# Performance work log

Measured on AMD Instinct MI355X. Metric: run time of the kernel, lower is better.

The kernel has to match this reference:

```python
import jax, jax.numpy as jnp
import numpy as np

N = 50000      # nodes
E = 800000     # edges (avg degree 16)
D_IN, D_H, D_OUT = 128, 256, 128


def setup_inputs() -> dict:
    key = jax.random.key(0)
    ks = jax.random.split(key, 12)
    x = jax.random.normal(ks[0], (N, D_IN), jnp.float32)
    src = jax.random.randint(ks[1], (E,), 0, N)
    dst = jax.random.randint(ks[2], (E,), 0, N)

    def lin(k, din, dout):
        return (jax.random.normal(k, (din, dout), jnp.float32) / np.sqrt(din)).astype(jnp.float32)

    dims = [(D_IN, D_H), (D_H, D_H), (D_H, D_OUT)]
    params = {}
    ki = 3
    for i, (di, do) in enumerate(dims):
        params[f"W_self{i}"] = lin(ks[ki], di, do); ki += 1
        params[f"W_neigh{i}"] = lin(ks[ki], di, do); ki += 1
        params[f"b{i}"] = jnp.zeros((do,), jnp.float32)
    return {"x": x, "src": src, "dst": dst, **params}


def _mean_agg(h, src, dst):
    # gather src features along edges, segment-mean into dst nodes
    msg = jnp.take(h, src, axis=0)                              # [E, D]
    s = jax.ops.segment_sum(msg, dst, num_segments=N)           # [N, D]
    deg = jax.ops.segment_sum(jnp.ones((dst.shape[0], 1), h.dtype), dst, num_segments=N)
    return s / jnp.maximum(deg, 1.0)                            # zero-degree -> 0, as in DGL


def reference(x, src, dst,
              W_self0, W_neigh0, b0,
              W_self1, W_neigh1, b1,
              W_self2, W_neigh2, b2):
    Ws = [(W_self0, W_neigh0, b0), (W_self1, W_neigh1, b1), (W_self2, W_neigh2, b2)]
    h = x
    for i, (Ws_i, Wn_i, b_i) in enumerate(Ws):
        neigh = _mean_agg(h, src, dst)
        h = h @ Ws_i + neigh @ Wn_i + b_i                       # SAGEConv('mean')
        if i < len(Ws) - 1:
            h = jax.nn.relu(h)                                  # activation between layers
    return h
```

## Files before the change

kernel.cpp:

```cpp
#include <hip/hip_runtime.h>

#define NN 50000
#define NE 800000
#define NCHK 200
#define CHKE 4000
#define NBUK 196
#define BCAP 5120
#define NOFF (NBUK * NCHK)
#define NSB  ((NOFF + 255) / 256)

typedef __attribute__((ext_vector_type(8))) short short8;
typedef __attribute__((ext_vector_type(4))) float f32x4;
typedef unsigned int u32;
typedef unsigned short u16;

__device__ __forceinline__ float bf2f(short u) {
    union { unsigned int i; float f; } c;
    c.i = ((unsigned int)(unsigned short)u) << 16;
    return c.f;
}
__device__ __forceinline__ short f2bf(float f) {
    union { float f; unsigned int i; } c; c.f = f;
    unsigned int u = c.i;
    unsigned int r = (u + 0x7FFFu + ((u >> 16) & 1u)) >> 16;
    return (short)r;
}


__global__ void cvt_f32_bf16_kernel(const float* __restrict__ in, short* __restrict__ out, int n) {
    int gid = blockIdx.x * 256 + threadIdx.x;
    if (gid < n) out[gid] = f2bf(in[gid]);
}

__global__ void wcvt_all_kernel(const float* __restrict__ Ws0, const float* __restrict__ Wn0,
                                const float* __restrict__ Ws1, const float* __restrict__ Wn1,
                                const float* __restrict__ Ws2, const float* __restrict__ Wn2,
                                short* __restrict__ wts) {
    int gid = blockIdx.x * 256 + threadIdx.x;
    const float* W; int K, Dout, base, loc;
    if (gid < 65536)       { K = 128; Dout = 256; base = (gid < 32768)  ? 0 : 32768;
                             W = (gid < 32768)  ? Ws0 : Wn0; loc = gid & 32767; }
    else if (gid < 196608) { K = 256; Dout = 256; base = (gid < 131072) ? 65536 : 131072;
                             W = (gid < 131072) ? Ws1 : Wn1; loc = (gid - 65536) & 65535; }
    else                   { K = 256; Dout = 128; base = (gid < 229376) ? 196608 : 229376;
                             W = (gid < 229376) ? Ws2 : Wn2; loc = (gid - 196608) & 32767; }
    int k = loc / Dout, d = loc - k * Dout;
    int kt = k >> 6, ks = (k >> 5) & 1, kg = (k >> 3) & 3, j = k & 7;
    int cgp = d >> 4, l = d & 15;
    int off = ((((kt * 2 + ks) * (Dout >> 4) + cgp) * 4 + kg) * 16 + l) * 8 + j;
    wts[base + off] = f2bf(W[(long)k * Dout + d]);
}

__global__ __launch_bounds__(256) void bucket_hist_kernel(const int* __restrict__ dst,
                                                          int* __restrict__ chist) {
    __shared__ int lh[NBUK];
    int b = blockIdx.x, t = threadIdx.x;
    for (int i = t; i < NBUK; i += 256) lh[i] = 0;
    __syncthreads();
    int base = b * CHKE;
    for (int i = t; i < CHKE; i += 256) atomicAdd(&lh[dst[base + i] >> 8], 1);
    __syncthreads();
    for (int i = t; i < NBUK; i += 256) chist[i * NCHK + b] = lh[i];
}

__global__ __launch_bounds__(256) void off_blocksum_kernel(const int* __restrict__ in,
                                                           int* __restrict__ bsum) {
    __shared__ int sm[256];
    int t = threadIdx.x;
    int idx = blockIdx.x * 256 + t;
    sm[t] = (idx < NOFF) ? in[idx] : 0;
    __syncthreads();
    for (int off = 128; off > 0; off >>= 1) {
        if (t < off) sm[t] += sm[t + off];
        __syncthreads();
    }
    if (t == 0) bsum[blockIdx.x] = sm[0];
}

__global__ __launch_bounds__(256) void off_scanb_kernel(const int* __restrict__ bsum,
                                                        int* __restrict__ bpre) {
    __shared__ int sm[256];
    int t = threadIdx.x;
    sm[t] = (t < NSB) ? bsum[t] : 0;
    __syncthreads();
    for (int o = 1; o < 256; o <<= 1) {
        int v = sm[t];
        int a = (t >= o) ? sm[t - o] : 0;
        __syncthreads();
        sm[t] = v + a;
        __syncthreads();
    }
    if (t < NSB) bpre[t] = (t == 0) ? 0 : sm[t - 1];
}

__global__ __launch_bounds__(256) void off_scatter_kernel(const int* __restrict__ in,
                                                          const int* __restrict__ bpre,
                                                          int* __restrict__ off) {
    __shared__ int sm[256];
    int t = threadIdx.x;
    int idx = blockIdx.x * 256 + t;
    int val = (idx < NOFF) ? in[idx] : 0;
    sm[t] = val;
    __syncthreads();
    for (int o = 1; o < 256; o <<= 1) {
        int v = sm[t];
        int a = (t >= o) ? sm[t - o] : 0;
        __syncthreads();
        sm[t] = v + a;
        __syncthreads();
    }
    if (idx < NOFF) off[idx] = bpre[blockIdx.x] + sm[t] - val;
}

__global__ __launch_bounds__(256) void bucket_scatter_kernel(const int* __restrict__ src,
                                                             const int* __restrict__ dst,
                                                             const int* __restrict__ off,
                                                             u32* __restrict__ ebuf) {
    __shared__ int lcur[NBUK];
    int b = blockIdx.x, t = threadIdx.x;
    for (int i = t; i < NBUK; i += 256) lcur[i] = off[i * NCHK + b];
    __syncthreads();
    int base = b * CHKE;
    for (int i = t; i < CHKE; i += 256) {
        int d = dst[base + i], s = src[base + i];
        int slot = atomicAdd(&lcur[d >> 8], 1);
        ebuf[slot] = ((u32)(d & 255) << 16) | (u32)s;
    }
}

__global__ __launch_bounds__(256) void bucket_sort_kernel(const u32* __restrict__ ebuf,
                                                          const int* __restrict__ off,
                                                          u16* __restrict__ srcs16,
                                                          int* __restrict__ row_start,
                                                          int* __restrict__ cnt) {
    __shared__ u32 earr[BCAP];
    __shared__ u16 s16[BCAP];
    __shared__ int lhist[256], lpre[256], lcur[256];
    int k = blockIdx.x, t = threadIdx.x;
    int base = off[k * NCHK];
    int end  = (k < NBUK - 1) ? off[(k + 1) * NCHK] : NE;
    int nE = end - base;
    lhist[t] = 0;
    __syncthreads();
    for (int i = t; i < nE; i += 256) {
        u32 e = ebuf[base + i];
        earr[i] = e;
        atomicAdd(&lhist[e >> 16], 1);
    }
    __syncthreads();
    int v = lhist[t];
    lpre[t] = v;
    __syncthreads();
    for (int o = 1; o < 256; o <<= 1) {
        int x = lpre[t];
        int a = (t >= o) ? lpre[t - o] : 0;
        __syncthreads();
        lpre[t] = x + a;
        __syncthreads();
    }
    int excl = lpre[t] - v;
    int node = k * 256 + t;
    if (node < NN) { row_start[node] = base + excl; cnt[node] = v; }
    lcur[t] = excl;
    __syncthreads();
    for (int i = t; i < nE; i += 256) {
        u32 e = earr[i];
        int pos = atomicAdd(&lcur[e >> 16], 1);
        s16[pos] = (u16)(e & 0xFFFFu);
    }
    __syncthreads();
    for (int i = t; i < nE; i += 256) srcs16[base + i] = s16[i];
}


template<int D>
__global__ __launch_bounds__(256) void gather_mean2_kernel(
    const short* __restrict__ h, const u16* __restrict__ srcs,
    const int* __restrict__ row_start, const int* __restrict__ cnt,
    short* __restrict__ nb)
{
    constexpr int CPR = D / 8;
    constexpr int EPL = 64 / CPR;
    const int wave = threadIdx.x >> 6;
    const int lane = threadIdx.x & 63;
    const int v = blockIdx.x * 4 + wave;
    if (v >= NN) return;
    const int c  = cnt[v];
    const int rs = row_start[v];
    const int slot = lane / CPR;
    const int cg   = lane & (CPR - 1);
    float acc[8];
    #pragma unroll
    for (int j = 0; j < 8; ++j) acc[j] = 0.f;
    const short8* hp = (const short8*)h;
    int i = slot;
    for (; i + 3 * EPL < c; i += 4 * EPL) {
        int s0 = srcs[rs + i];
        int s1 = srcs[rs + i + EPL];
        int s2 = srcs[rs + i + 2 * EPL];
        int s3 = srcs[rs + i + 3 * EPL];
        short8 v0 = hp[(size_t)s0 * CPR + cg];
        short8 v1 = hp[(size_t)s1 * CPR + cg];
        short8 v2 = hp[(size_t)s2 * CPR + cg];
        short8 v3 = hp[(size_t)s3 * CPR + cg];
        #pragma unroll
        for (int j = 0; j < 8; ++j)
            acc[j] += (bf2f(v0[j]) + bf2f(v1[j])) + (bf2f(v2[j]) + bf2f(v3[j]));
    }
    for (; i < c; i += EPL) {
        int s0 = srcs[rs + i];
        short8 v0 = hp[(size_t)s0 * CPR + cg];
        #pragma unroll
        for (int j = 0; j < 8; ++j) acc[j] += bf2f(v0[j]);
    }
    #pragma unroll
    for (int j = 0; j < 8; ++j) {
        if (EPL == 4) acc[j] += __shfl_xor(acc[j], 16);
        acc[j] += __shfl_xor(acc[j], 32);
    }
    if (slot == 0) {
        float inv = (c > 0) ? (1.0f / (float)c) : 0.0f;
        short8 outv;
        #pragma unroll
        for (int j = 0; j < 8; ++j) outv[j] = f2bf(acc[j] * inv);
        ((short8*)nb)[(size_t)v * CPR + cg] = outv;
    }
}

template<int NOUT, int KK, int PHASES, bool RELU, bool OUT_F32, bool ADDIN, bool BIAS>
__global__ __launch_bounds__(512, 2) void gemm_sage4_kernel(
    const short* __restrict__ Aself, const short* __restrict__ Aneigh,
    const short* __restrict__ Bself, const short* __restrict__ Bneigh,
    const float* __restrict__ bias, void* __restrict__ outp, int M,
    const short* __restrict__ addin)
{
    constexpr int WN = NOUT / 64;
    constexpr int WM = 8 / WN;
    constexpr int MR = 128 / (WM * 16);
    constexpr int NR = 4;
    constexpr int KT = KK / 64;
    constexpr int NT = PHASES * KT;
    constexpr int CG = NOUT / 16;

    __shared__ short ldsA[2][128 * 64];

    const int tid  = threadIdx.x;
    const int wave = tid >> 6;
    const int lane = tid & 63;
    const int wm = wave / WN;
    const int wn = wave % WN;
    const int l15 = lane & 15;
    const int kg  = lane >> 4;
    const int bm  = blockIdx.x * 128;

    f32x4 acc[MR][NR];
    #pragma unroll
    for (int a = 0; a < MR; ++a)
        #pragma unroll
        for (int b = 0; b < NR; ++b)
            acc[a][b] = (f32x4){0.f, 0.f, 0.f, 0.f};

    const int srow = tid >> 3;
    const int scol = ((tid & 7) << 3) ^ ((srow & 7) << 3);

    auto stageA = [&](int buf, int t) {
        int ph = t / KT, kt = t - ph * KT;
        const short* A = ph ? Aneigh : Aself;
        #pragma unroll
        for (int c = 0; c < 2; ++c) {
            const short* gp = A + (size_t)(bm + c * 64 + srow) * KK + kt * 64 + scol;
            __builtin_amdgcn_global_load_lds(
                (const __attribute__((address_space(1))) u32*)gp,
                (__attribute__((address_space(3))) u32*)(&ldsA[buf][c * 4096 + (wave << 9)]),
                16, 0, 0);
        }
    };

    stageA(0, 0);
    __syncthreads();

    #pragma unroll
    for (int ph = 0; ph < PHASES; ++ph) {
        const short* __restrict__ Wb = ph ? Bneigh : Bself;
        short8 wreg[KT][2][NR];
        #pragma unroll
        for (int kt = 0; kt < KT; ++kt)
            #pragma unroll
            for (int ks = 0; ks < 2; ++ks)
                #pragma unroll
                for (int nr = 0; nr < NR; ++nr)
                    wreg[kt][ks][nr] = *(const short8*)(
                        Wb + (size_t)((((kt * 2 + ks) * CG + wn * 4 + nr) * 4 + kg) * 16 + l15) * 8);

        #pragma unroll
        for (int kt = 0; kt < KT; ++kt) {
            const int t = ph * KT + kt;
            const int cur = t & 1;
            if (t + 1 < NT) stageA(cur ^ 1, t + 1);

            #pragma unroll
            for (int ks = 0; ks < 2; ++ks) {
                short8 areg[MR];
                #pragma unroll
                for (int mr = 0; mr < MR; ++mr) {
                    int r = wm * (MR * 16) + mr * 16 + l15;
                    areg[mr] = *(const short8*)(&ldsA[cur][r * 64 + ((ks * 32 + kg * 8) ^ ((r & 7) << 3))]);
                }
                #pragma unroll
                for (int mr = 0; mr < MR; ++mr)
                    #pragma unroll
                    for (int nr = 0; nr < NR; ++nr)
                        acc[mr][nr] = __builtin_amdgcn_mfma_f32_16x16x32_bf16(
                            areg[mr], wreg[kt][ks][nr], acc[mr][nr], 0, 0, 0);
            }
            __syncthreads();
        }
    }

    #pragma unroll
    for (int mr = 0; mr < MR; ++mr) {
        int rowb = bm + wm * (MR * 16) + mr * 16 + kg * 4;
        #pragma unroll
        for (int nr = 0; nr < NR; ++nr) {
            int col = wn * 64 + nr * 16 + l15;
            float bv = BIAS ? bias[col] : 0.f;
            #pragma unroll
            for (int r = 0; r < 4; ++r) {
                int row = rowb + r;
                if (row < M) {
                    float vv = acc[mr][nr][r] + bv;
                    if (ADDIN) vv += bf2f(addin[(size_t)row * NOUT + col]);
                    if (RELU) vv = fmaxf(vv, 0.f);
                    if (OUT_F32) ((float*)outp)[(size_t)row * NOUT + col] = vv;
                    else         ((short*)outp)[(size_t)row * NOUT + col] = f2bf(vv);
                }
            }
        }
    }
}


extern "C" void kernel_launch(void* const* d_in, const int* in_sizes, int n_in,
                              void* d_out, int out_size, void* d_ws, size_t ws_size,
                              hipStream_t stream) {
    const float* x    = (const float*)d_in[0];
    const int*   srcp = (const int*)d_in[1];
    const int*   dstp = (const int*)d_in[2];
    const float* Ws0  = (const float*)d_in[3];
    const float* Wn0  = (const float*)d_in[4];
    const float* b0   = (const float*)d_in[5];
    const float* Ws1  = (const float*)d_in[6];
    const float* Wn1  = (const float*)d_in[7];
    const float* b1   = (const float*)d_in[8];
    const float* Ws2  = (const float*)d_in[9];
    const float* Wn2  = (const float*)d_in[10];
    const float* b2   = (const float*)d_in[11];

    char* base = (char*)d_ws;
    size_t off_b = 0;
    auto alloc = [&](size_t bytes) -> void* {
        void* p = base + off_b;
        off_b += (bytes + 255) & ~(size_t)255;
        return p;
    };

    int*   cnt       = (int*)alloc((size_t)NN * 4);
    int*   row_start = (int*)alloc((size_t)NN * 4);
    int*   chist     = (int*)alloc((size_t)NOFF * 4);
    int*   offb      = (int*)alloc((size_t)NOFF * 4);
    int*   bsum      = (int*)alloc((size_t)NSB * 4);
    int*   bpre      = (int*)alloc((size_t)NSB * 4);
    u32*   ebuf      = (u32*)alloc((size_t)NE * 4);
    u16*   srcs16    = (u16*)alloc((size_t)NE * 2);
    short* hA        = (short*)alloc((size_t)NN * 256 * 2);
    short* hB        = (short*)alloc((size_t)NN * 256 * 2);
    short* nb        = (short*)alloc((size_t)NN * 256 * 2);
    short* wts       = (short*)alloc((size_t)262144 * 2 + 65536);
    short* Wt0s = wts;
    short* Wt0n = Wt0s + 32768;
    short* Wt1s = Wt0n + 32768;
    short* Wt1n = Wt1s + 65536;
    short* Wt2s = Wt1n + 65536;
    short* Wt2n = Wt2s + 32768;

    bucket_hist_kernel<<<NCHK, 256, 0, stream>>>(dstp, chist);
    off_blocksum_kernel<<<NSB, 256, 0, stream>>>(chist, bsum);
    off_scanb_kernel<<<1, 256, 0, stream>>>(bsum, bpre);
    off_scatter_kernel<<<NSB, 256, 0, stream>>>(chist, bpre, offb);
    bucket_scatter_kernel<<<NCHK, 256, 0, stream>>>(srcp, dstp, offb, ebuf);
    bucket_sort_kernel<<<NBUK, 256, 0, stream>>>(ebuf, offb, srcs16, row_start, cnt);

    wcvt_all_kernel<<<1024, 256, 0, stream>>>(Ws0, Wn0, Ws1, Wn1, Ws2, Wn2, wts);

    cvt_f32_bf16_kernel<<<(NN * 128 + 255) / 256, 256, 0, stream>>>(x, hA, NN * 128);

    const int mblocks = (NN + 127) / 128;
    const int gblocks = (NN + 3) / 4;

    gather_mean2_kernel<128><<<gblocks, 256, 0, stream>>>(hA, srcs16, row_start, cnt, nb);
    gemm_sage4_kernel<256, 128, 2, true, false, false, true><<<mblocks, 512, 0, stream>>>(
        hA, nb, Wt0s, Wt0n, b0, hB, NN, nullptr);

    gather_mean2_kernel<256><<<gblocks, 256, 0, stream>>>(hB, srcs16, row_start, cnt, nb);
    gemm_sage4_kernel<256, 256, 2, true, false, false, true><<<mblocks, 512, 0, stream>>>(
        hB, nb, Wt1s, Wt1n, b1, hA, NN, nullptr);

    gemm_sage4_kernel<128, 256, 1, false, false, false, false><<<mblocks, 512, 0, stream>>>(
        hA, hA, Wt2n, Wt2n, nullptr, hB, NN, nullptr);
    gather_mean2_kernel<128><<<gblocks, 256, 0, stream>>>(hB, srcs16, row_start, cnt, nb);
    gemm_sage4_kernel<128, 256, 1, false, true, true, true><<<mblocks, 512, 0, stream>>>(
        hA, hA, Wt2s, Wt2s, b2, d_out, NN, nb);
}
```

Baseline: 246.8 us.

## Shrink GEMM blocks to 256 threads and stream weight fragments per k-step

The SAGE GEMM drops from 512-thread, 128-row tiles to 256-thread tiles (64 rows for the 256-wide layers, 128 rows for the 128-wide ones). Each wave now always computes a 4x4 MFMA tile. Weight fragments are no longer preloaded in registers for a whole phase; they are loaded from global memory for each k-step inside a single flat loop over phases. The aim is to cut register pressure and raise occupancy (launch bounds 256,4). The cost is more repeated weight loads from cache and, for the 256-wide layers, twice as many blocks that each re-read the weights.

```diff
diff --git a/kernel.cpp b/kernel.cpp
--- a/kernel.cpp
+++ b/kernel.cpp
@@ -228,21 +228,23 @@
 }
 
 template<int NOUT, int KK, int PHASES, bool RELU, bool OUT_F32, bool ADDIN, bool BIAS>
-__global__ __launch_bounds__(512, 2) void gemm_sage4_kernel(
+__global__ __launch_bounds__(256, 4) void gemm_sage5_kernel(
     const short* __restrict__ Aself, const short* __restrict__ Aneigh,
     const short* __restrict__ Bself, const short* __restrict__ Bneigh,
     const float* __restrict__ bias, void* __restrict__ outp, int M,
     const short* __restrict__ addin)
 {
     constexpr int WN = NOUT / 64;
-    constexpr int WM = 8 / WN;
-    constexpr int MR = 128 / (WM * 16);
+    constexpr int WM = 4 / WN;
+    constexpr int BM = 64 * WM;
+    constexpr int SC = BM / 32;
+    constexpr int MR = 4;
     constexpr int NR = 4;
     constexpr int KT = KK / 64;
     constexpr int NT = PHASES * KT;
     constexpr int CG = NOUT / 16;
 
-    __shared__ short ldsA[2][128 * 64];
+    __shared__ short ldsA[2][BM * 64];
 
     const int tid  = threadIdx.x;
     const int wave = tid >> 6;
@@ -251,7 +253,7 @@
     const int wn = wave % WN;
     const int l15 = lane & 15;
     const int kg  = lane >> 4;
-    const int bm  = blockIdx.x * 128;
+    const int bm  = blockIdx.x * BM;
 
     f32x4 acc[MR][NR];
     #pragma unroll
@@ -267,11 +269,11 @@
         int ph = t / KT, kt = t - ph * KT;
         const short* A = ph ? Aneigh : Aself;
         #pragma unroll
-        for (int c = 0; c < 2; ++c) {
-            const short* gp = A + (size_t)(bm + c * 64 + srow) * KK + kt * 64 + scol;
+        for (int c = 0; c < SC; ++c) {
+            const short* gp = A + (size_t)(bm + c * 32 + srow) * KK + kt * 64 + scol;
             __builtin_amdgcn_global_load_lds(
                 (const __attribute__((address_space(1))) u32*)gp,
-                (__attribute__((address_space(3))) u32*)(&ldsA[buf][c * 4096 + (wave << 9)]),
+                (__attribute__((address_space(3))) u32*)(&ldsA[buf][c * 2048 + (wave << 9)]),
                 16, 0, 0);
         }
     };
@@ -279,47 +281,38 @@
     stageA(0, 0);
     __syncthreads();
 
-    #pragma unroll
-    for (int ph = 0; ph < PHASES; ++ph) {
+    for (int t = 0; t < NT; ++t) {
+        const int cur = t & 1;
+        if (t + 1 < NT) stageA(cur ^ 1, t + 1);
+        const int ph = t / KT, kt = t - ph * KT;
         const short* __restrict__ Wb = ph ? Bneigh : Bself;
-        short8 wreg[KT][2][NR];
-        #pragma unroll
-        for (int kt = 0; kt < KT; ++kt)
+
+        #pragma unroll
+        for (int ks = 0; ks < 2; ++ks) {
+            short8 wreg[NR];
             #pragma unroll
-            for (int ks = 0; ks < 2; ++ks)
+            for (int nr = 0; nr < NR; ++nr)
+                wreg[nr] = *(const short8*)(
+                    Wb + (size_t)((((kt * 2 + ks) * CG + wn * NR + nr) * 4 + kg) * 16 + l15) * 8);
+            short8 areg[MR];
+            #pragma unroll
+            for (int mr = 0; mr < MR; ++mr) {
+                int r = wm * 64 + mr * 16 + l15;
+                areg[mr] = *(const short8*)(&ldsA[cur][r * 64 + ((ks * 32 + kg * 8) ^ ((r & 7) << 3))]);
+            }
+            #pragma unroll
+            for (int mr = 0; mr < MR; ++mr)
                 #pragma unroll
                 for (int nr = 0; nr < NR; ++nr)
-                    wreg[kt][ks][nr] = *(const short8*)(
-                        Wb + (size_t)((((kt * 2 + ks) * CG + wn * 4 + nr) * 4 + kg) * 16 + l15) * 8);
-
-        #pragma unroll
-        for (int kt = 0; kt < KT; ++kt) {
-            const int t = ph * KT + kt;
-            const int cur = t & 1;
-            if (t + 1 < NT) stageA(cur ^ 1, t + 1);
-
-            #pragma unroll
-            for (int ks = 0; ks < 2; ++ks) {
-                short8 areg[MR];
-                #pragma unroll
-                for (int mr = 0; mr < MR; ++mr) {
-                    int r = wm * (MR * 16) + mr * 16 + l15;
-                    areg[mr] = *(const short8*)(&ldsA[cur][r * 64 + ((ks * 32 + kg * 8) ^ ((r & 7) << 3))]);
-                }
-                #pragma unroll
-                for (int mr = 0; mr < MR; ++mr)
-                    #pragma unroll
-                    for (int nr = 0; nr < NR; ++nr)
-                        acc[mr][nr] = __builtin_amdgcn_mfma_f32_16x16x32_bf16(
-                            areg[mr], wreg[kt][ks][nr], acc[mr][nr], 0, 0, 0);
-            }
-            __syncthreads();
+                    acc[mr][nr] = __builtin_amdgcn_mfma_f32_16x16x32_bf16(
+                        areg[mr], wreg[nr], acc[mr][nr], 0, 0, 0);
         }
+        __syncthreads();
     }
 
     #pragma unroll
     for (int mr = 0; mr < MR; ++mr) {
-        int rowb = bm + wm * (MR * 16) + mr * 16 + kg * 4;
+        int rowb = bm + wm * 64 + mr * 16 + kg * 4;
         #pragma unroll
         for (int nr = 0; nr < NR; ++nr) {
             int col = wn * 64 + nr * 16 + l15;
@@ -394,20 +387,21 @@
 
     cvt_f32_bf16_kernel<<<(NN * 128 + 255) / 256, 256, 0, stream>>>(x, hA, NN * 128);
 
-    const int mblocks = (NN + 127) / 128;
+    const int mblk64  = (NN + 63) / 64;
+    const int mblk128 = (NN + 127) / 128;
     const int gblocks = (NN + 3) / 4;
 
     gather_mean2_kernel<128><<<gblocks, 256, 0, stream>>>(hA, srcs16, row_start, cnt, nb);
-    gemm_sage4_kernel<256, 128, 2, true, false, false, true><<<mblocks, 512, 0, stream>>>(
+    gemm_sage5_kernel<256, 128, 2, true, false, false, true><<<mblk64, 256, 0, stream>>>(
         hA, nb, Wt0s, Wt0n, b0, hB, NN, nullptr);
 
     gather_mean2_kernel<256><<<gblocks, 256, 0, stream>>>(hB, srcs16, row_start, cnt, nb);
-    gemm_sage4_kernel<256, 256, 2, true, false, false, true><<<mblocks, 512, 0, stream>>>(
+    gemm_sage5_kernel<256, 256, 2, true, false, false, true><<<mblk64, 256, 0, stream>>>(
         hB, nb, Wt1s, Wt1n, b1, hA, NN, nullptr);
 
-    gemm_sage4_kernel<128, 256, 1, false, false, false, false><<<mblocks, 512, 0, stream>>>(
+    gemm_sage5_kernel<128, 256, 1, false, false, false, false><<<mblk128, 256, 0, stream>>>(
         hA, hA, Wt2n, Wt2n, nullptr, hB, NN, nullptr);
     gather_mean2_kernel<128><<<gblocks, 256, 0, stream>>>(hB, srcs16, row_start, cnt, nb);
-    gemm_sage4_kernel<128, 256, 1, false, true, true, true><<<mblocks, 512, 0, stream>>>(
+    gemm_sage5_kernel<128, 256, 1, false, true, true, true><<<mblk128, 256, 0, stream>>>(
         hA, hA, Wt2s, Wt2s, b2, d_out, NN, nb);
 }
```

Result: faster. 236.1 us (-4.3%).
